# Performance work log

Measured on AMD Instinct MI355X. Metric: run time of the kernel, lower is better.

## Reference

```python
import jax, jax.numpy as jnp
import numpy as np

N = 100000
E = 3200000
IN_DIM = 128
OUT_DIM = 64


def setup_inputs() -> dict:
    key = jax.random.key(0)
    k1, k2, k3, k4, k5, k6 = jax.random.split(key, 6)
    x = jax.random.normal(k1, (N, IN_DIM), dtype=jnp.float32)
    edge_index = jax.random.randint(k2, (2, E), 0, N, dtype=jnp.int64)
    edge_weight = jax.random.uniform(k3, (E,), dtype=jnp.float32)
    # Learned params: Linear weight (in->out, no bias), attention vectors a_src/a_tgt
    limit_w = float(np.sqrt(1.0 / IN_DIM))
    W = jax.random.uniform(k4, (IN_DIM, OUT_DIM), minval=-limit_w, maxval=limit_w, dtype=jnp.float32)
    # xavier_uniform for (out_dim, 1) parameters
    limit_a = float(np.sqrt(6.0 / (OUT_DIM + 1)))
    a_src = jax.random.uniform(k5, (OUT_DIM,), minval=-limit_a, maxval=limit_a, dtype=jnp.float32)
    a_tgt = jax.random.uniform(k6, (OUT_DIM,), minval=-limit_a, maxval=limit_a, dtype=jnp.float32)
    return {"x": x, "edge_index": edge_index, "edge_weight": edge_weight,
            "W": W, "a_src": a_src, "a_tgt": a_tgt}


def reference(x, edge_index, edge_weight, W, a_src, a_tgt):
    n = x.shape[0]
    h = x @ W  # (N, out_dim)
    src, tgt = edge_index[0], edge_index[1]
    # per-node attention logits, gathered per edge
    hs = h @ a_src  # (N,)
    ht = h @ a_tgt  # (N,)
    e = jax.nn.leaky_relu(hs[src] + ht[tgt], negative_slope=0.2)  # (E,)
    e = e * edge_weight
    # segment softmax over incoming edges of each target node
    e_max = jax.ops.segment_max(e, tgt, num_segments=n)  # (N,), -inf for isolated nodes
    e_exp = jnp.exp(e - e_max[tgt])  # (E,)
    e_sum = jax.ops.segment_sum(e_exp, tgt, num_segments=n)  # (N,)
    alpha = e_exp / (e_sum[tgt] + 1e-10)  # (E,)
    # weighted scatter-add aggregation
    out = jax.ops.segment_sum(alpha[:, None] * h[src], tgt, num_segments=n)  # (N, out_dim)
    return out
```

## Files before the change

### kernel.cpp

```cpp
#include <hip/hip_runtime.h>


#define IN_DIM 128
#define OUT_DIM 64
#define MAXBKT 512
#define BKN 256
#define SEPT 8
#define SCHUNK (1024 * SEPT)
#define CAP 9216

typedef __attribute__((ext_vector_type(8))) short bf16x8;
typedef __attribute__((ext_vector_type(4))) float f32x4;

__device__ __forceinline__ unsigned short f2bf(float f) {
    unsigned u = __float_as_uint(f);
    return (unsigned short)((u + 0x7FFFu + ((u >> 16) & 1u)) >> 16);
}
__device__ __forceinline__ float bf2f(unsigned short u) {
    return __uint_as_float((unsigned)u << 16);
}

__device__ __forceinline__ float expg(float d) {
    return __expf(fmaxf(d, -80.f));
}

__global__ __launch_bounds__(256) void k_linear(
    const float* __restrict__ x, const float* __restrict__ W,
    const float* __restrict__ a_src, const float* __restrict__ a_tgt,
    unsigned short* __restrict__ hh, float* __restrict__ hs,
    float* __restrict__ ht, int n)
{
    __shared__ unsigned short xhi[64][136];
    __shared__ unsigned short xlo[64][136];
    __shared__ unsigned short whi[64][136];
    __shared__ unsigned short wlo[64][136];
    const int tid   = threadIdx.x;
    const int node0 = blockIdx.x * 64;

    {
        const float4* W4 = (const float4*)W;
        #pragma unroll
        for (int j = 0; j < 8; ++j) {
            int i4 = tid + 256 * j;
            int k = i4 >> 4, d4 = i4 & 15;
            float4 v = W4[i4];
            float vv[4] = {v.x, v.y, v.z, v.w};
            #pragma unroll
            for (int m = 0; m < 4; ++m) {
                unsigned short hi = f2bf(vv[m]);
                float lo = vv[m] - bf2f(hi);
                whi[d4 * 4 + m][k] = hi;
                wlo[d4 * 4 + m][k] = f2bf(lo);
            }
        }
    }
    {
        #pragma unroll
        for (int j = 0; j < 8; ++j) {
            int i4 = tid + 256 * j;
            int r = i4 >> 5, c4 = i4 & 31;
            int node = node0 + r;
            float4 v = make_float4(0.f, 0.f, 0.f, 0.f);
            if (node < n) v = ((const float4*)(x + (size_t)node * IN_DIM))[c4];
            float vv[4] = {v.x, v.y, v.z, v.w};
            ushort4 ph, pl;
            unsigned short* php = (unsigned short*)&ph;
            unsigned short* plp = (unsigned short*)&pl;
            #pragma unroll
            for (int m = 0; m < 4; ++m) {
                unsigned short hi = f2bf(vv[m]);
                php[m] = hi;
                plp[m] = f2bf(vv[m] - bf2f(hi));
            }
            *(ushort4*)&xhi[r][c4 * 4] = ph;
            *(ushort4*)&xlo[r][c4 * 4] = pl;
        }
    }
    __syncthreads();

    const int l15  = tid & 15;
    const int lhi  = (tid & 63) >> 4;
    const int wv   = tid >> 6;
    const int arow = wv * 16 + l15;
    const int kb   = lhi * 8;

    bf16x8 ahi[4], alo[4];
    #pragma unroll
    for (int k0 = 0; k0 < 4; ++k0) {
        ahi[k0] = *(const bf16x8*)&xhi[arow][k0 * 32 + kb];
        alo[k0] = *(const bf16x8*)&xlo[arow][k0 * 32 + kb];
    }

    f32x4 acc[4];
    #pragma unroll
    for (int ntt = 0; ntt < 4; ++ntt) acc[ntt] = (f32x4){0.f, 0.f, 0.f, 0.f};

    #pragma unroll
    for (int ntt = 0; ntt < 4; ++ntt) {
        #pragma unroll
        for (int k0 = 0; k0 < 4; ++k0) {
            bf16x8 bhi = *(const bf16x8*)&whi[ntt * 16 + l15][k0 * 32 + kb];
            bf16x8 blo = *(const bf16x8*)&wlo[ntt * 16 + l15][k0 * 32 + kb];
            acc[ntt] = __builtin_amdgcn_mfma_f32_16x16x32_bf16(ahi[k0], bhi, acc[ntt], 0, 0, 0);
            acc[ntt] = __builtin_amdgcn_mfma_f32_16x16x32_bf16(ahi[k0], blo, acc[ntt], 0, 0, 0);
            acc[ntt] = __builtin_amdgcn_mfma_f32_16x16x32_bf16(alo[k0], bhi, acc[ntt], 0, 0, 0);
        }
    }

    float asv[4], atv[4];
    #pragma unroll
    for (int ntt = 0; ntt < 4; ++ntt) {
        asv[ntt] = a_src[ntt * 16 + l15];
        atv[ntt] = a_tgt[ntt * 16 + l15];
    }
    #pragma unroll
    for (int q = 0; q < 4; ++q) {
        float ps = 0.f, pt = 0.f;
        #pragma unroll
        for (int ntt = 0; ntt < 4; ++ntt) {
            ps += acc[ntt][q] * asv[ntt];
            pt += acc[ntt][q] * atv[ntt];
        }
        #pragma unroll
        for (int off = 8; off; off >>= 1) {
            ps += __shfl_xor(ps, off);
            pt += __shfl_xor(pt, off);
        }
        int node = node0 + wv * 16 + lhi * 4 + q;
        if (l15 == 0 && node < n) { hs[node] = ps; ht[node] = pt; }
    }

    __syncthreads();
    #pragma unroll
    for (int ntt = 0; ntt < 4; ++ntt) {
        #pragma unroll
        for (int q = 0; q < 4; ++q) {
            xhi[wv * 16 + lhi * 4 + q][ntt * 16 + l15] = f2bf(acc[ntt][q]);
        }
    }
    __syncthreads();
    #pragma unroll
    for (int j = 0; j < 4; ++j) {
        int i = tid + 256 * j;
        int r = i >> 4, c4 = i & 15;
        int node = node0 + r;
        if (node < n) {
            ushort4 v = *(const ushort4*)&xhi[r][c4 * 4];
            ((ushort4*)(hh + (size_t)node * OUT_DIM))[c4] = v;
        }
    }
}

__global__ __launch_bounds__(1024) void k_count(
    const int* __restrict__ tgt, int* __restrict__ histT,
    int ecount, int nbkt, int nsb)
{
    __shared__ int h[MAXBKT];
    const int tid = threadIdx.x;
    const int e0  = blockIdx.x * SCHUNK;
    for (int i = tid; i < nbkt; i += 1024) h[i] = 0;
    __syncthreads();
    #pragma unroll
    for (int k = 0; k < SEPT; ++k) {
        int j = e0 + k * 1024 + tid;
        if (j < ecount) atomicAdd(&h[tgt[j] >> 8], 1);
    }
    __syncthreads();
    for (int i = tid; i < nbkt; i += 1024) histT[i * nsb + blockIdx.x] = h[i];
}

__global__ __launch_bounds__(512) void k_colscan(
    int* __restrict__ histT, int* __restrict__ bfill, int nsb)
{
    __shared__ int lds[512];
    const int bkt = blockIdx.x;
    const int tid = threadIdx.x;
    int v = (tid < nsb) ? histT[bkt * nsb + tid] : 0;
    lds[tid] = v;
    __syncthreads();
    for (int off = 1; off < 512; off <<= 1) {
        int u = (tid >= off) ? lds[tid - off] : 0;
        __syncthreads();
        lds[tid] += u;
        __syncthreads();
    }
    int excl = lds[tid] - v;
    if (tid < nsb) histT[bkt * nsb + tid] = bkt * CAP + excl;
    if (tid == 511) bfill[bkt] = bkt * CAP + lds[511];
}

__global__ __launch_bounds__(1024) void k_scat(
    const int* __restrict__ src, const int* __restrict__ tgt,
    const float* __restrict__ ew, const float* __restrict__ hs,
    const float* __restrict__ ht, const int* __restrict__ histT,
    float2* __restrict__ ecoarse, int ecount, int nbkt, int nsb)
{
    __shared__ int h[MAXBKT];
    __shared__ int base[MAXBKT];
    const int tid = threadIdx.x;
    const int e0  = blockIdx.x * SCHUNK;

    for (int i = tid; i < nbkt; i += 1024) {
        h[i] = 0;
        base[i] = histT[i * nsb + blockIdx.x];
    }

    unsigned kreg[SEPT]; int breg[SEPT]; float wreg[SEPT];
    #pragma unroll
    for (int k = 0; k < SEPT; ++k) {
        int j = e0 + k * 1024 + tid;
        bool valid = j < ecount;
        int s = valid ? src[j] : 0;
        int t = valid ? tgt[j] : 0;
        wreg[k] = valid ? ew[j] : 0.f;
        kreg[k] = ((unsigned)s << 8) | ((unsigned)t & 255u);
        breg[k] = t >> 8;
    }
    float hsr[SEPT], htr[SEPT];
    #pragma unroll
    for (int k = 0; k < SEPT; ++k) hsr[k] = hs[kreg[k] >> 8];
    #pragma unroll
    for (int k = 0; k < SEPT; ++k) htr[k] = ht[(breg[k] << 8) | (int)(kreg[k] & 255u)];

    __syncthreads();

    int rank[SEPT];
    #pragma unroll
    for (int k = 0; k < SEPT; ++k) {
        int j = e0 + k * 1024 + tid;
        if (j < ecount) rank[k] = atomicAdd(&h[breg[k]], 1);
    }

    #pragma unroll
    for (int k = 0; k < SEPT; ++k) {
        int j = e0 + k * 1024 + tid;
        if (j < ecount) {
            float v = hsr[k] + htr[k];
            v = (v > 0.f) ? v : 0.2f * v;
            v *= wreg[k];
            ecoarse[base[breg[k]] + rank[k]] = make_float2(__uint_as_float(kreg[k]), v);
        }
    }
}

__global__ __launch_bounds__(1024, 8) void k_bucket(
    const int* __restrict__ bfill, const float2* __restrict__ ecoarse,
    const unsigned short* __restrict__ hh, float* __restrict__ out, int n)
{
    __shared__ float2 recs[CAP];
    __shared__ int   cnt[BKN];
    __shared__ int   pos0[BKN];
    __shared__ int   fill[BKN];
    __shared__ float mf[BKN];
    __shared__ float rden[BKN];

    const int tid   = threadIdx.x;
    const int bkt   = blockIdx.x;
    const int base  = bkt * CAP;
    const int node0 = bkt << 8;
    const int mcnt  = bfill[bkt] - base;

    for (int i = tid; i < BKN; i += 1024) cnt[i] = 0;
    __syncthreads();

    for (int j = tid; j < mcnt; j += 1024) {
        unsigned k = __float_as_uint(ecoarse[base + j].x);
        atomicAdd(&cnt[k & 255u], 1);
    }
    __syncthreads();

    if (tid < BKN) pos0[tid] = cnt[tid];
    __syncthreads();
    for (int off = 1; off < BKN; off <<= 1) {
        int u = 0;
        if (tid < BKN && tid >= off) u = pos0[tid - off];
        __syncthreads();
        if (tid < BKN) pos0[tid] += u;
        __syncthreads();
    }
    if (tid < BKN) fill[tid] = pos0[tid] - cnt[tid];
    __syncthreads();
    if (tid < BKN) pos0[tid] = fill[tid];
    __syncthreads();

    for (int j = tid; j < mcnt; j += 1024) {
        float2 e = ecoarse[base + j];
        unsigned k = __float_as_uint(e.x);
        int p = atomicAdd(&fill[k & 255u], 1);
        recs[p] = e;
    }
    __syncthreads();

    {
        const int G   = tid >> 4;
        const int l16 = tid & 15;
        #pragma unroll
        for (int r = 0; r < 4; ++r) {
            int tl = G + 64 * r;
            int s0 = pos0[tl], c = cnt[tl];
            float m = -INFINITY, s = 0.f;
            for (int j = l16; j < c; j += 16) {
                float v = recs[s0 + j].y;
                float nm = fmaxf(m, v);
                s = s * expg(m - nm) + expg(v - nm);
                m = nm;
            }
            #pragma unroll
            for (int off = 8; off; off >>= 1) {
                float mo = __shfl_xor(m, off);
                float so = __shfl_xor(s, off);
                float nm = fmaxf(m, mo);
                s = s * expg(m - nm) + so * expg(mo - nm);
                m = nm;
            }
            if (l16 == 0) { mf[tl] = m; rden[tl] = 1.f / (s + 1e-10f); }
        }
    }
    __syncthreads();

    const int lane = tid & 63;
    const int wv   = tid >> 6;
    const int g    = lane >> 4;
    const int l4   = lane & 15;
    #pragma unroll 1
    for (int r = 0; r < 16; ++r) {
        int tl = wv + 16 * r;
        int node = node0 + tl;
        if (node >= n) continue;
        int s0 = pos0[tl], e_ = s0 + cnt[tl];
        float m = mf[tl], rd = rden[tl];
        float4 a0 = make_float4(0.f, 0.f, 0.f, 0.f);
        float4 a1 = make_float4(0.f, 0.f, 0.f, 0.f);
        int j = s0;
        for (; j + 8 <= e_; j += 8) {
            float2 e0 = recs[j + g];
            float2 e1 = recs[j + 4 + g];
            int sA = (int)(__float_as_uint(e0.x) >> 8);
            int sB = (int)(__float_as_uint(e1.x) >> 8);
            ushort4 u0 = ((const ushort4*)(hh + (size_t)sA * OUT_DIM))[l4];
            ushort4 u1 = ((const ushort4*)(hh + (size_t)sB * OUT_DIM))[l4];
            float c0 = __expf(e0.y - m) * rd;
            float c1 = __expf(e1.y - m) * rd;
            a0.x += c0 * bf2f(u0.x); a0.y += c0 * bf2f(u0.y);
            a0.z += c0 * bf2f(u0.z); a0.w += c0 * bf2f(u0.w);
            a1.x += c1 * bf2f(u1.x); a1.y += c1 * bf2f(u1.y);
            a1.z += c1 * bf2f(u1.z); a1.w += c1 * bf2f(u1.w);
        }
        for (; j < e_; j += 4) {
            int jj = j + g;
            bool valid = jj < e_;
            float2 ed = recs[valid ? jj : (e_ - 1)];
            int sidx = (int)(__float_as_uint(ed.x) >> 8);
            ushort4 uv = ((const ushort4*)(hh + (size_t)sidx * OUT_DIM))[l4];
            float c = valid ? __expf(ed.y - m) * rd : 0.f;
            a0.x += c * bf2f(uv.x); a0.y += c * bf2f(uv.y);
            a0.z += c * bf2f(uv.z); a0.w += c * bf2f(uv.w);
        }
        a0.x += a1.x; a0.y += a1.y; a0.z += a1.z; a0.w += a1.w;

        #pragma unroll
        for (int off = 32; off >= 16; off >>= 1) {
            a0.x += __shfl_xor(a0.x, off);
            a0.y += __shfl_xor(a0.y, off);
            a0.z += __shfl_xor(a0.z, off);
            a0.w += __shfl_xor(a0.w, off);
        }
        if (g == 0)
            ((float4*)(out + (size_t)node * OUT_DIM))[l4] = a0;
    }
}

extern "C" void kernel_launch(void* const* d_in, const int* in_sizes, int n_in,
                              void* d_out, int out_size, void* d_ws, size_t ws_size,
                              hipStream_t stream) {
    const float* x     = (const float*)d_in[0];
    const int*   eidx  = (const int*)d_in[1];
    const float* ew    = (const float*)d_in[2];
    const float* W     = (const float*)d_in[3];
    const float* a_src = (const float*)d_in[4];
    const float* a_tgt = (const float*)d_in[5];
    float* out = (float*)d_out;

    const int n = in_sizes[0] / IN_DIM;
    const int E = in_sizes[2];
    const int* src = eidx;
    const int* tgt = eidx + E;
    const int nbkt = (n + BKN - 1) / BKN;
    const int nsb  = (E + SCHUNK - 1) / SCHUNK;

    unsigned* ws = (unsigned*)d_ws;
    unsigned short* hh = (unsigned short*)ws;  ws += (size_t)n * OUT_DIM / 2;
    float* hs     = (float*)ws;          ws += n;
    float* ht     = (float*)ws;          ws += n;
    int*   bfill  = (int*)ws;            ws += MAXBKT;
    int*   histT  = (int*)ws;            ws += (size_t)nbkt * nsb;
    ws = (unsigned*)(((uintptr_t)ws + 7) & ~(uintptr_t)7);
    float2* ecoarse = (float2*)ws;

    k_linear<<<(n + 63) / 64, 256, 0, stream>>>(x, W, a_src, a_tgt, hh, hs, ht, n);
    k_count<<<nsb, 1024, 0, stream>>>(tgt, histT, E, nbkt, nsb);
    k_colscan<<<nbkt, 512, 0, stream>>>(histT, bfill, nsb);
    k_scat<<<nsb, 1024, 0, stream>>>(src, tgt, ew, hs, ht, histT, ecoarse, E, nbkt, nsb);
    k_bucket<<<nbkt, 1024, 0, stream>>>(bfill, ecoarse, hh, out, n);
}
```

Measured before the change: 271.3 us.

## Split each bucket across two half-blocks and precompute normalized softmax coefficients

```diff
diff --git a/kernel.cpp b/kernel.cpp
--- a/kernel.cpp
+++ b/kernel.cpp
@@ -5,9 +5,11 @@
 #define OUT_DIM 64
 #define MAXBKT 512
 #define BKN 256
+#define HBKN 128
 #define SEPT 8
 #define SCHUNK (1024 * SEPT)
 #define CAP 9216
+#define CAPL 4736
 
 typedef __attribute__((ext_vector_type(8))) short bf16x8;
 typedef __attribute__((ext_vector_type(4))) float f32x4;
@@ -243,51 +245,55 @@
     }
 }
 
-__global__ __launch_bounds__(1024, 8) void k_bucket(
+__global__ __launch_bounds__(512, 8) void k_half(
     const int* __restrict__ bfill, const float2* __restrict__ ecoarse,
     const unsigned short* __restrict__ hh, float* __restrict__ out, int n)
 {
-    __shared__ float2 recs[CAP];
-    __shared__ int   cnt[BKN];
-    __shared__ int   pos0[BKN];
-    __shared__ int   fill[BKN];
-    __shared__ float mf[BKN];
-    __shared__ float rden[BKN];
+    __shared__ float2 recs[CAPL];
+    __shared__ int   cnt[HBKN];
+    __shared__ int   pos0[HBKN];
+    __shared__ int   fill[HBKN];
+    __shared__ float mf[HBKN];
+    __shared__ float rden[HBKN];
 
     const int tid   = threadIdx.x;
-    const int bkt   = blockIdx.x;
+    const int B     = blockIdx.x;
+    const int bkt   = B >> 1;
+    const int hf    = B & 1;
     const int base  = bkt * CAP;
-    const int node0 = bkt << 8;
+    const int node0 = (bkt << 8) + (hf << 7);
     const int mcnt  = bfill[bkt] - base;
 
-    for (int i = tid; i < BKN; i += 1024) cnt[i] = 0;
-    __syncthreads();
-
-    for (int j = tid; j < mcnt; j += 1024) {
-        unsigned k = __float_as_uint(ecoarse[base + j].x);
-        atomicAdd(&cnt[k & 255u], 1);
-    }
-    __syncthreads();
-
-    if (tid < BKN) pos0[tid] = cnt[tid];
-    __syncthreads();
-    for (int off = 1; off < BKN; off <<= 1) {
+    for (int i = tid; i < HBKN; i += 512) cnt[i] = 0;
+    __syncthreads();
+
+    for (int j = tid; j < mcnt; j += 512) {
+        int tl = (int)(__float_as_uint(ecoarse[base + j].x) & 255u);
+        if ((tl >> 7) == hf) atomicAdd(&cnt[tl & 127], 1);
+    }
+    __syncthreads();
+
+    if (tid < HBKN) pos0[tid] = cnt[tid];
+    __syncthreads();
+    for (int off = 1; off < HBKN; off <<= 1) {
         int u = 0;
-        if (tid < BKN && tid >= off) u = pos0[tid - off];
+        if (tid < HBKN && tid >= off) u = pos0[tid - off];
         __syncthreads();
-        if (tid < BKN) pos0[tid] += u;
+        if (tid < HBKN) pos0[tid] += u;
         __syncthreads();
     }
-    if (tid < BKN) fill[tid] = pos0[tid] - cnt[tid];
-    __syncthreads();
-    if (tid < BKN) pos0[tid] = fill[tid];
-    __syncthreads();
-
-    for (int j = tid; j < mcnt; j += 1024) {
+    if (tid < HBKN) fill[tid] = pos0[tid] - cnt[tid];
+    __syncthreads();
+    if (tid < HBKN) pos0[tid] = fill[tid];
+    __syncthreads();
+
+    for (int j = tid; j < mcnt; j += 512) {
         float2 e = ecoarse[base + j];
-        unsigned k = __float_as_uint(e.x);
-        int p = atomicAdd(&fill[k & 255u], 1);
-        recs[p] = e;
+        int tl = (int)(__float_as_uint(e.x) & 255u);
+        if ((tl >> 7) == hf) {
+            int p = atomicAdd(&fill[tl & 127], 1);
+            if (p < CAPL) recs[p] = e;
+        }
     }
     __syncthreads();
 
@@ -296,7 +302,7 @@
         const int l16 = tid & 15;
         #pragma unroll
         for (int r = 0; r < 4; ++r) {
-            int tl = G + 64 * r;
+            int tl = G + 32 * r;
             int s0 = pos0[tl], c = cnt[tl];
             float m = -INFINITY, s = 0.f;
             for (int j = l16; j < c; j += 16) {
@@ -318,17 +324,25 @@
     }
     __syncthreads();
 
+    int ntot = fill[HBKN - 1];
+    if (ntot > CAPL) ntot = CAPL;
+    for (int j = tid; j < ntot; j += 512) {
+        float2 e = recs[j];
+        int tl = (int)(__float_as_uint(e.x) & 127u);
+        recs[j].y = __expf(e.y - mf[tl]) * rden[tl];
+    }
+    __syncthreads();
+
     const int lane = tid & 63;
     const int wv   = tid >> 6;
     const int g    = lane >> 4;
     const int l4   = lane & 15;
     #pragma unroll 1
     for (int r = 0; r < 16; ++r) {
-        int tl = wv + 16 * r;
+        int tl = wv + 8 * r;
         int node = node0 + tl;
         if (node >= n) continue;
         int s0 = pos0[tl], e_ = s0 + cnt[tl];
-        float m = mf[tl], rd = rden[tl];
         float4 a0 = make_float4(0.f, 0.f, 0.f, 0.f);
         float4 a1 = make_float4(0.f, 0.f, 0.f, 0.f);
         int j = s0;
@@ -339,8 +353,8 @@
             int sB = (int)(__float_as_uint(e1.x) >> 8);
             ushort4 u0 = ((const ushort4*)(hh + (size_t)sA * OUT_DIM))[l4];
             ushort4 u1 = ((const ushort4*)(hh + (size_t)sB * OUT_DIM))[l4];
-            float c0 = __expf(e0.y - m) * rd;
-            float c1 = __expf(e1.y - m) * rd;
+            float c0 = e0.y;
+            float c1 = e1.y;
             a0.x += c0 * bf2f(u0.x); a0.y += c0 * bf2f(u0.y);
             a0.z += c0 * bf2f(u0.z); a0.w += c0 * bf2f(u0.w);
             a1.x += c1 * bf2f(u1.x); a1.y += c1 * bf2f(u1.y);
@@ -352,7 +366,7 @@
             float2 ed = recs[valid ? jj : (e_ - 1)];
             int sidx = (int)(__float_as_uint(ed.x) >> 8);
             ushort4 uv = ((const ushort4*)(hh + (size_t)sidx * OUT_DIM))[l4];
-            float c = valid ? __expf(ed.y - m) * rd : 0.f;
+            float c = valid ? ed.y : 0.f;
             a0.x += c * bf2f(uv.x); a0.y += c * bf2f(uv.y);
             a0.z += c * bf2f(uv.z); a0.w += c * bf2f(uv.w);
         }
@@ -401,5 +415,5 @@
     k_count<<<nsb, 1024, 0, stream>>>(tgt, histT, E, nbkt, nsb);
     k_colscan<<<nbkt, 512, 0, stream>>>(histT, bfill, nsb);
     k_scat<<<nsb, 1024, 0, stream>>>(src, tgt, ew, hs, ht, histT, ecoarse, E, nbkt, nsb);
-    k_bucket<<<nbkt, 1024, 0, stream>>>(bfill, ecoarse, hh, out, n);
-}
+    k_half<<<2 * nbkt, 512, 0, stream>>>(bfill, ecoarse, hh, out, n);
+}
```

Result: slower. 278.5 us (+2.6%).

## Fuse all graph-attention stages into one cooperative persistent kernel with grid syncs

Applied to the files above, without the earlier changes.

```diff
diff --git a/kernel.cpp b/kernel.cpp
--- a/kernel.cpp
+++ b/kernel.cpp
@@ -1,4 +1,7 @@
 #include <hip/hip_runtime.h>
+#include <hip/hip_cooperative_groups.h>
+
+namespace cg = cooperative_groups;
 
 
 #define IN_DIM 128
@@ -19,275 +22,244 @@
 __device__ __forceinline__ float bf2f(unsigned short u) {
     return __uint_as_float((unsigned)u << 16);
 }
-
 __device__ __forceinline__ float expg(float d) {
     return __expf(fmaxf(d, -80.f));
 }
 
-__global__ __launch_bounds__(256) void k_linear(
-    const float* __restrict__ x, const float* __restrict__ W,
-    const float* __restrict__ a_src, const float* __restrict__ a_tgt,
-    unsigned short* __restrict__ hh, float* __restrict__ hs,
-    float* __restrict__ ht, int n)
-{
-    __shared__ unsigned short xhi[64][136];
-    __shared__ unsigned short xlo[64][136];
-    __shared__ unsigned short whi[64][136];
-    __shared__ unsigned short wlo[64][136];
-    const int tid   = threadIdx.x;
-    const int node0 = blockIdx.x * 64;
-
-    {
-        const float4* W4 = (const float4*)W;
-        #pragma unroll
-        for (int j = 0; j < 8; ++j) {
-            int i4 = tid + 256 * j;
+struct KParams {
+    const float* x; const float* W; const float* a_src; const float* a_tgt;
+    const int* src; const int* tgt; const float* ew;
+    unsigned short* hh; float* hs; float* ht;
+    int* bfill; int* histT; float2* ecoarse; float* out;
+    int n, ecount, nbkt, nsb, nlb;
+};
+
+union SharedU {
+    struct {
+        unsigned short whi[64][136], wlo[64][136];
+        unsigned short xhi[64][136], xlo[64][136];
+        float hsp[4][64], htp[4][64];
+    } lin;
+    struct { int h[MAXBKT]; int base[MAXBKT]; } cs;
+    struct { int lds[512]; } scan;
+    struct {
+        float2 recs[CAP];
+        int cnt[BKN], pos0[BKN], fill[BKN];
+        float mf[BKN], rden[BKN];
+    } bkt;
+};
+
+__device__ void phase_lin(const KParams& P, SharedU& su, int blk, int tid)
+{
+    auto& L = su.lin;
+    if (blk < P.nlb) {
+        const float4* W4 = (const float4*)P.W;
+        #pragma unroll
+        for (int j = 0; j < 2; ++j) {
+            int i4 = tid + 1024 * j;
             int k = i4 >> 4, d4 = i4 & 15;
             float4 v = W4[i4];
             float vv[4] = {v.x, v.y, v.z, v.w};
             #pragma unroll
             for (int m = 0; m < 4; ++m) {
                 unsigned short hi = f2bf(vv[m]);
-                float lo = vv[m] - bf2f(hi);
-                whi[d4 * 4 + m][k] = hi;
-                wlo[d4 * 4 + m][k] = f2bf(lo);
-            }
-        }
-    }
-    {
-        #pragma unroll
-        for (int j = 0; j < 8; ++j) {
-            int i4 = tid + 256 * j;
-            int r = i4 >> 5, c4 = i4 & 31;
-            int node = node0 + r;
-            float4 v = make_float4(0.f, 0.f, 0.f, 0.f);
-            if (node < n) v = ((const float4*)(x + (size_t)node * IN_DIM))[c4];
-            float vv[4] = {v.x, v.y, v.z, v.w};
-            ushort4 ph, pl;
-            unsigned short* php = (unsigned short*)&ph;
-            unsigned short* plp = (unsigned short*)&pl;
+                L.whi[d4 * 4 + m][k] = hi;
+                L.wlo[d4 * 4 + m][k] = f2bf(vv[m] - bf2f(hi));
+            }
+        }
+    }
+    const int lane = tid & 63, l15 = lane & 15, lhi = lane >> 4;
+    const int w = tid >> 6, rowgrp = w & 3, nt = w >> 2;
+    const int arow = rowgrp * 16 + l15, kb = lhi * 8;
+
+    for (int tt = 0; tt < 4; ++tt) {
+        const int node0 = blk * 256 + tt * 64;
+        const bool act = (blk < P.nlb) && (node0 < P.n);
+        __syncthreads();
+        if (act) {
             #pragma unroll
-            for (int m = 0; m < 4; ++m) {
-                unsigned short hi = f2bf(vv[m]);
-                php[m] = hi;
-                plp[m] = f2bf(vv[m] - bf2f(hi));
-            }
-            *(ushort4*)&xhi[r][c4 * 4] = ph;
-            *(ushort4*)&xlo[r][c4 * 4] = pl;
-        }
-    }
-    __syncthreads();
-
-    const int l15  = tid & 15;
-    const int lhi  = (tid & 63) >> 4;
-    const int wv   = tid >> 6;
-    const int arow = wv * 16 + l15;
-    const int kb   = lhi * 8;
-
-    bf16x8 ahi[4], alo[4];
-    #pragma unroll
-    for (int k0 = 0; k0 < 4; ++k0) {
-        ahi[k0] = *(const bf16x8*)&xhi[arow][k0 * 32 + kb];
-        alo[k0] = *(const bf16x8*)&xlo[arow][k0 * 32 + kb];
-    }
-
-    f32x4 acc[4];
-    #pragma unroll
-    for (int ntt = 0; ntt < 4; ++ntt) acc[ntt] = (f32x4){0.f, 0.f, 0.f, 0.f};
-
-    #pragma unroll
-    for (int ntt = 0; ntt < 4; ++ntt) {
-        #pragma unroll
-        for (int k0 = 0; k0 < 4; ++k0) {
-            bf16x8 bhi = *(const bf16x8*)&whi[ntt * 16 + l15][k0 * 32 + kb];
-            bf16x8 blo = *(const bf16x8*)&wlo[ntt * 16 + l15][k0 * 32 + kb];
-            acc[ntt] = __builtin_amdgcn_mfma_f32_16x16x32_bf16(ahi[k0], bhi, acc[ntt], 0, 0, 0);
-            acc[ntt] = __builtin_amdgcn_mfma_f32_16x16x32_bf16(ahi[k0], blo, acc[ntt], 0, 0, 0);
-            acc[ntt] = __builtin_amdgcn_mfma_f32_16x16x32_bf16(alo[k0], bhi, acc[ntt], 0, 0, 0);
-        }
-    }
-
-    float asv[4], atv[4];
-    #pragma unroll
-    for (int ntt = 0; ntt < 4; ++ntt) {
-        asv[ntt] = a_src[ntt * 16 + l15];
-        atv[ntt] = a_tgt[ntt * 16 + l15];
-    }
-    #pragma unroll
-    for (int q = 0; q < 4; ++q) {
-        float ps = 0.f, pt = 0.f;
-        #pragma unroll
-        for (int ntt = 0; ntt < 4; ++ntt) {
-            ps += acc[ntt][q] * asv[ntt];
-            pt += acc[ntt][q] * atv[ntt];
-        }
-        #pragma unroll
-        for (int off = 8; off; off >>= 1) {
-            ps += __shfl_xor(ps, off);
-            pt += __shfl_xor(pt, off);
-        }
-        int node = node0 + wv * 16 + lhi * 4 + q;
-        if (l15 == 0 && node < n) { hs[node] = ps; ht[node] = pt; }
-    }
-
-    __syncthreads();
-    #pragma unroll
-    for (int ntt = 0; ntt < 4; ++ntt) {
-        #pragma unroll
-        for (int q = 0; q < 4; ++q) {
-            xhi[wv * 16 + lhi * 4 + q][ntt * 16 + l15] = f2bf(acc[ntt][q]);
-        }
-    }
-    __syncthreads();
-    #pragma unroll
-    for (int j = 0; j < 4; ++j) {
-        int i = tid + 256 * j;
-        int r = i >> 4, c4 = i & 15;
-        int node = node0 + r;
-        if (node < n) {
-            ushort4 v = *(const ushort4*)&xhi[r][c4 * 4];
-            ((ushort4*)(hh + (size_t)node * OUT_DIM))[c4] = v;
-        }
-    }
-}
-
-__global__ __launch_bounds__(1024) void k_count(
-    const int* __restrict__ tgt, int* __restrict__ histT,
-    int ecount, int nbkt, int nsb)
-{
-    __shared__ int h[MAXBKT];
-    const int tid = threadIdx.x;
-    const int e0  = blockIdx.x * SCHUNK;
-    for (int i = tid; i < nbkt; i += 1024) h[i] = 0;
-    __syncthreads();
+            for (int j = 0; j < 2; ++j) {
+                int i4 = tid + 1024 * j;
+                int r = i4 >> 5, c4 = i4 & 31;
+                int node = node0 + r;
+                float4 v = make_float4(0.f, 0.f, 0.f, 0.f);
+                if (node < P.n) v = ((const float4*)(P.x + (size_t)node * IN_DIM))[c4];
+                float vv[4] = {v.x, v.y, v.z, v.w};
+                ushort4 ph, pl;
+                unsigned short* php = (unsigned short*)&ph;
+                unsigned short* plp = (unsigned short*)&pl;
+                #pragma unroll
+                for (int m = 0; m < 4; ++m) {
+                    unsigned short hi = f2bf(vv[m]);
+                    php[m] = hi;
+                    plp[m] = f2bf(vv[m] - bf2f(hi));
+                }
+                *(ushort4*)&L.xhi[r][c4 * 4] = ph;
+                *(ushort4*)&L.xlo[r][c4 * 4] = pl;
+            }
+        }
+        __syncthreads();
+        if (act) {
+            f32x4 acc = (f32x4){0.f, 0.f, 0.f, 0.f};
+            #pragma unroll
+            for (int k0 = 0; k0 < 4; ++k0) {
+                bf16x8 ahi = *(const bf16x8*)&L.xhi[arow][k0 * 32 + kb];
+                bf16x8 alo = *(const bf16x8*)&L.xlo[arow][k0 * 32 + kb];
+                bf16x8 bhi = *(const bf16x8*)&L.whi[nt * 16 + l15][k0 * 32 + kb];
+                bf16x8 blo = *(const bf16x8*)&L.wlo[nt * 16 + l15][k0 * 32 + kb];
+                acc = __builtin_amdgcn_mfma_f32_16x16x32_bf16(ahi, bhi, acc, 0, 0, 0);
+                acc = __builtin_amdgcn_mfma_f32_16x16x32_bf16(ahi, blo, acc, 0, 0, 0);
+                acc = __builtin_amdgcn_mfma_f32_16x16x32_bf16(alo, bhi, acc, 0, 0, 0);
+            }
+            float asv = P.a_src[nt * 16 + l15];
+            float atv = P.a_tgt[nt * 16 + l15];
+            #pragma unroll
+            for (int q = 0; q < 4; ++q) {
+                float ps = acc[q] * asv, pt = acc[q] * atv;
+                #pragma unroll
+                for (int off = 8; off; off >>= 1) {
+                    ps += __shfl_xor(ps, off);
+                    pt += __shfl_xor(pt, off);
+                }
+                int rit = rowgrp * 16 + lhi * 4 + q;
+                if (l15 == 0) { L.hsp[nt][rit] = ps; L.htp[nt][rit] = pt; }
+                int node = node0 + rit;
+                if (node < P.n)
+                    P.hh[(size_t)node * OUT_DIM + nt * 16 + l15] = f2bf(acc[q]);
+            }
+        }
+        __syncthreads();
+        if (act && tid < 64) {
+            int node = node0 + tid;
+            if (node < P.n) {
+                P.hs[node] = L.hsp[0][tid] + L.hsp[1][tid] + L.hsp[2][tid] + L.hsp[3][tid];
+                P.ht[node] = L.htp[0][tid] + L.htp[1][tid] + L.htp[2][tid] + L.htp[3][tid];
+            }
+        }
+    }
+}
+
+__device__ void phase_count(const KParams& P, SharedU& su, int blk, int tid)
+{
+    if (blk >= P.nsb) return;
+    auto& C = su.cs;
+    for (int i = tid; i < P.nbkt; i += 1024) C.h[i] = 0;
+    __syncthreads();
+    const int e0 = blk * SCHUNK;
     #pragma unroll
     for (int k = 0; k < SEPT; ++k) {
         int j = e0 + k * 1024 + tid;
-        if (j < ecount) atomicAdd(&h[tgt[j] >> 8], 1);
-    }
-    __syncthreads();
-    for (int i = tid; i < nbkt; i += 1024) histT[i * nsb + blockIdx.x] = h[i];
-}
-
-__global__ __launch_bounds__(512) void k_colscan(
-    int* __restrict__ histT, int* __restrict__ bfill, int nsb)
-{
-    __shared__ int lds[512];
-    const int bkt = blockIdx.x;
-    const int tid = threadIdx.x;
-    int v = (tid < nsb) ? histT[bkt * nsb + tid] : 0;
-    lds[tid] = v;
+        if (j < P.ecount) atomicAdd(&C.h[P.tgt[j] >> 8], 1);
+    }
+    __syncthreads();
+    for (int i = tid; i < P.nbkt; i += 1024) P.histT[i * P.nsb + blk] = C.h[i];
+}
+
+__device__ void phase_scan(const KParams& P, SharedU& su, int blk, int tid)
+{
+    if (blk >= P.nbkt) return;
+    int v = 0;
+    if (tid < 512) {
+        v = (tid < P.nsb) ? P.histT[blk * P.nsb + tid] : 0;
+        su.scan.lds[tid] = v;
+    }
     __syncthreads();
     for (int off = 1; off < 512; off <<= 1) {
-        int u = (tid >= off) ? lds[tid - off] : 0;
-        __syncthreads();
-        lds[tid] += u;
-        __syncthreads();
-    }
-    int excl = lds[tid] - v;
-    if (tid < nsb) histT[bkt * nsb + tid] = bkt * CAP + excl;
-    if (tid == 511) bfill[bkt] = bkt * CAP + lds[511];
-}
-
-__global__ __launch_bounds__(1024) void k_scat(
-    const int* __restrict__ src, const int* __restrict__ tgt,
-    const float* __restrict__ ew, const float* __restrict__ hs,
-    const float* __restrict__ ht, const int* __restrict__ histT,
-    float2* __restrict__ ecoarse, int ecount, int nbkt, int nsb)
-{
-    __shared__ int h[MAXBKT];
-    __shared__ int base[MAXBKT];
-    const int tid = threadIdx.x;
-    const int e0  = blockIdx.x * SCHUNK;
-
-    for (int i = tid; i < nbkt; i += 1024) {
-        h[i] = 0;
-        base[i] = histT[i * nsb + blockIdx.x];
-    }
-
-    unsigned kreg[SEPT]; int breg[SEPT]; float wreg[SEPT];
-    #pragma unroll
-    for (int k = 0; k < SEPT; ++k) {
-        int j = e0 + k * 1024 + tid;
-        bool valid = j < ecount;
-        int s = valid ? src[j] : 0;
-        int t = valid ? tgt[j] : 0;
-        wreg[k] = valid ? ew[j] : 0.f;
-        kreg[k] = ((unsigned)s << 8) | ((unsigned)t & 255u);
-        breg[k] = t >> 8;
-    }
-    float hsr[SEPT], htr[SEPT];
-    #pragma unroll
-    for (int k = 0; k < SEPT; ++k) hsr[k] = hs[kreg[k] >> 8];
-    #pragma unroll
-    for (int k = 0; k < SEPT; ++k) htr[k] = ht[(breg[k] << 8) | (int)(kreg[k] & 255u)];
-
-    __syncthreads();
-
-    int rank[SEPT];
-    #pragma unroll
-    for (int k = 0; k < SEPT; ++k) {
-        int j = e0 + k * 1024 + tid;
-        if (j < ecount) rank[k] = atomicAdd(&h[breg[k]], 1);
-    }
-
-    #pragma unroll
-    for (int k = 0; k < SEPT; ++k) {
-        int j = e0 + k * 1024 + tid;
-        if (j < ecount) {
-            float v = hsr[k] + htr[k];
-            v = (v > 0.f) ? v : 0.2f * v;
-            v *= wreg[k];
-            ecoarse[base[breg[k]] + rank[k]] = make_float2(__uint_as_float(kreg[k]), v);
-        }
-    }
-}
-
-__global__ __launch_bounds__(1024, 8) void k_bucket(
-    const int* __restrict__ bfill, const float2* __restrict__ ecoarse,
-    const unsigned short* __restrict__ hh, float* __restrict__ out, int n)
-{
-    __shared__ float2 recs[CAP];
-    __shared__ int   cnt[BKN];
-    __shared__ int   pos0[BKN];
-    __shared__ int   fill[BKN];
-    __shared__ float mf[BKN];
-    __shared__ float rden[BKN];
-
-    const int tid   = threadIdx.x;
-    const int bkt   = blockIdx.x;
-    const int base  = bkt * CAP;
-    const int node0 = bkt << 8;
-    const int mcnt  = bfill[bkt] - base;
-
-    for (int i = tid; i < BKN; i += 1024) cnt[i] = 0;
+        int u = (tid < 512 && tid >= off) ? su.scan.lds[tid - off] : 0;
+        __syncthreads();
+        if (tid < 512) su.scan.lds[tid] += u;
+        __syncthreads();
+    }
+    if (tid < P.nsb) P.histT[blk * P.nsb + tid] = blk * CAP + (su.scan.lds[tid] - v);
+    if (tid == 511) P.bfill[blk] = blk * CAP + su.scan.lds[511];
+}
+
+__device__ void phase_scat(const KParams& P, SharedU& su, int blk, int tid)
+{
+    if (blk >= P.nsb) return;
+    auto& C = su.cs;
+    for (int i = tid; i < P.nbkt; i += 1024) {
+        C.h[i] = 0;
+        C.base[i] = P.histT[i * P.nsb + blk];
+    }
+    __syncthreads();
+    const int e0 = blk * SCHUNK;
+    #pragma unroll 1
+    for (int half = 0; half < 2; ++half) {
+        const int eh = e0 + half * 4096;
+        unsigned kreg[4]; int breg[4]; float wreg[4];
+        #pragma unroll
+        for (int k = 0; k < 4; ++k) {
+            int j = eh + k * 1024 + tid;
+            bool valid = j < P.ecount;
+            int s = valid ? P.src[j] : 0;
+            int t = valid ? P.tgt[j] : 0;
+            wreg[k] = valid ? P.ew[j] : 0.f;
+            kreg[k] = ((unsigned)s << 8) | ((unsigned)t & 255u);
+            breg[k] = t >> 8;
+        }
+        float hsr[4], htr[4];
+        #pragma unroll
+        for (int k = 0; k < 4; ++k) hsr[k] = P.hs[kreg[k] >> 8];
+        #pragma unroll
+        for (int k = 0; k < 4; ++k) htr[k] = P.ht[(breg[k] << 8) | (int)(kreg[k] & 255u)];
+        int rank[4];
+        #pragma unroll
+        for (int k = 0; k < 4; ++k) {
+            int j = eh + k * 1024 + tid;
+            if (j < P.ecount) rank[k] = atomicAdd(&C.h[breg[k]], 1);
+        }
+        #pragma unroll
+        for (int k = 0; k < 4; ++k) {
+            int j = eh + k * 1024 + tid;
+            if (j < P.ecount) {
+                float v = hsr[k] + htr[k];
+                v = (v > 0.f) ? v : 0.2f * v;
+                v *= wreg[k];
+                P.ecoarse[C.base[breg[k]] + rank[k]] =
+                    make_float2(__uint_as_float(kreg[k]), v);
+            }
+        }
+    }
+}
+
+__device__ void phase_bkt(const KParams& P, SharedU& su, int blk, int tid)
+{
+    if (blk >= P.nbkt) return;
+    auto& B = su.bkt;
+    const int base  = blk * CAP;
+    const int node0 = blk << 8;
+    int mcnt = P.bfill[blk] - base;
+    if (mcnt > CAP) mcnt = CAP;
+
+    for (int i = tid; i < BKN; i += 1024) B.cnt[i] = 0;
     __syncthreads();
 
     for (int j = tid; j < mcnt; j += 1024) {
-        unsigned k = __float_as_uint(ecoarse[base + j].x);
-        atomicAdd(&cnt[k & 255u], 1);
-    }
-    __syncthreads();
-
-    if (tid < BKN) pos0[tid] = cnt[tid];
+        unsigned k = __float_as_uint(P.ecoarse[base + j].x);
+        atomicAdd(&B.cnt[k & 255u], 1);
+    }
+    __syncthreads();
+
+    if (tid < BKN) B.pos0[tid] = B.cnt[tid];
     __syncthreads();
     for (int off = 1; off < BKN; off <<= 1) {
         int u = 0;
-        if (tid < BKN && tid >= off) u = pos0[tid - off];
-        __syncthreads();
-        if (tid < BKN) pos0[tid] += u;
-        __syncthreads();
-    }
-    if (tid < BKN) fill[tid] = pos0[tid] - cnt[tid];
-    __syncthreads();
-    if (tid < BKN) pos0[tid] = fill[tid];
+        if (tid < BKN && tid >= off) u = B.pos0[tid - off];
+        __syncthreads();
+        if (tid < BKN) B.pos0[tid] += u;
+        __syncthreads();
+    }
+    if (tid < BKN) B.fill[tid] = B.pos0[tid] - B.cnt[tid];
+    __syncthreads();
+    if (tid < BKN) B.pos0[tid] = B.fill[tid];
     __syncthreads();
 
     for (int j = tid; j < mcnt; j += 1024) {
-        float2 e = ecoarse[base + j];
+        float2 e = P.ecoarse[base + j];
         unsigned k = __float_as_uint(e.x);
-        int p = atomicAdd(&fill[k & 255u], 1);
-        recs[p] = e;
+        int p = atomicAdd(&B.fill[k & 255u], 1);
+        if (p < CAP) B.recs[p] = e;
     }
     __syncthreads();
 
@@ -297,10 +269,10 @@
         #pragma unroll
         for (int r = 0; r < 4; ++r) {
             int tl = G + 64 * r;
-            int s0 = pos0[tl], c = cnt[tl];
+            int s0 = B.pos0[tl], c = B.cnt[tl];
             float m = -INFINITY, s = 0.f;
             for (int j = l16; j < c; j += 16) {
-                float v = recs[s0 + j].y;
+                float v = B.recs[s0 + j].y;
                 float nm = fmaxf(m, v);
                 s = s * expg(m - nm) + expg(v - nm);
                 m = nm;
@@ -313,8 +285,17 @@
                 s = s * expg(m - nm) + so * expg(mo - nm);
                 m = nm;
             }
-            if (l16 == 0) { mf[tl] = m; rden[tl] = 1.f / (s + 1e-10f); }
-        }
+            if (l16 == 0) { B.mf[tl] = m; B.rden[tl] = 1.f / (s + 1e-10f); }
+        }
+    }
+    __syncthreads();
+
+    int ntot = B.fill[BKN - 1];
+    if (ntot > CAP) ntot = CAP;
+    for (int j = tid; j < ntot; j += 1024) {
+        float2 e = B.recs[j];
+        int tl = (int)(__float_as_uint(e.x) & 255u);
+        B.recs[j].y = __expf(e.y - B.mf[tl]) * B.rden[tl];
     }
     __syncthreads();
 
@@ -326,21 +307,19 @@
     for (int r = 0; r < 16; ++r) {
         int tl = wv + 16 * r;
         int node = node0 + tl;
-        if (node >= n) continue;
-        int s0 = pos0[tl], e_ = s0 + cnt[tl];
-        float m = mf[tl], rd = rden[tl];
+        if (node >= P.n) continue;
+        int s0 = B.pos0[tl], e_ = s0 + B.cnt[tl];
         float4 a0 = make_float4(0.f, 0.f, 0.f, 0.f);
         float4 a1 = make_float4(0.f, 0.f, 0.f, 0.f);
         int j = s0;
         for (; j + 8 <= e_; j += 8) {
-            float2 e0 = recs[j + g];
-            float2 e1 = recs[j + 4 + g];
+            float2 e0 = B.recs[j + g];
+            float2 e1 = B.recs[j + 4 + g];
             int sA = (int)(__float_as_uint(e0.x) >> 8);
             int sB = (int)(__float_as_uint(e1.x) >> 8);
-            ushort4 u0 = ((const ushort4*)(hh + (size_t)sA * OUT_DIM))[l4];
-            ushort4 u1 = ((const ushort4*)(hh + (size_t)sB * OUT_DIM))[l4];
-            float c0 = __expf(e0.y - m) * rd;
-            float c1 = __expf(e1.y - m) * rd;
+            ushort4 u0 = ((const ushort4*)(P.hh + (size_t)sA * OUT_DIM))[l4];
+            ushort4 u1 = ((const ushort4*)(P.hh + (size_t)sB * OUT_DIM))[l4];
+            float c0 = e0.y, c1 = e1.y;
             a0.x += c0 * bf2f(u0.x); a0.y += c0 * bf2f(u0.y);
             a0.z += c0 * bf2f(u0.z); a0.w += c0 * bf2f(u0.w);
             a1.x += c1 * bf2f(u1.x); a1.y += c1 * bf2f(u1.y);
@@ -349,15 +328,14 @@
         for (; j < e_; j += 4) {
             int jj = j + g;
             bool valid = jj < e_;
-            float2 ed = recs[valid ? jj : (e_ - 1)];
+            float2 ed = B.recs[valid ? jj : (e_ - 1)];
             int sidx = (int)(__float_as_uint(ed.x) >> 8);
-            ushort4 uv = ((const ushort4*)(hh + (size_t)sidx * OUT_DIM))[l4];
-            float c = valid ? __expf(ed.y - m) * rd : 0.f;
+            ushort4 uv = ((const ushort4*)(P.hh + (size_t)sidx * OUT_DIM))[l4];
+            float c = valid ? ed.y : 0.f;
             a0.x += c * bf2f(uv.x); a0.y += c * bf2f(uv.y);
             a0.z += c * bf2f(uv.z); a0.w += c * bf2f(uv.w);
         }
         a0.x += a1.x; a0.y += a1.y; a0.z += a1.z; a0.w += a1.w;
-
         #pragma unroll
         for (int off = 32; off >= 16; off >>= 1) {
             a0.x += __shfl_xor(a0.x, off);
@@ -366,9 +344,34 @@
             a0.w += __shfl_xor(a0.w, off);
         }
         if (g == 0)
-            ((float4*)(out + (size_t)node * OUT_DIM))[l4] = a0;
-    }
-}
+            ((float4*)(P.out + (size_t)node * OUT_DIM))[l4] = a0;
+    }
+}
+
+__global__ __launch_bounds__(1024, 8) void k_fused(KParams P)
+{
+    __shared__ SharedU su;
+    cg::grid_group grid = cg::this_grid();
+    const int tid = threadIdx.x;
+    const int blk = blockIdx.x;
+
+    phase_lin(P, su, blk, tid);
+    __syncthreads();
+    phase_count(P, su, blk, tid);
+    grid.sync();
+    phase_scan(P, su, blk, tid);
+    grid.sync();
+    phase_scat(P, su, blk, tid);
+    grid.sync();
+    __syncthreads();
+    phase_bkt(P, su, blk, tid);
+}
+
+__global__ __launch_bounds__(1024, 8) void k_p0(KParams P) { __shared__ SharedU su; phase_lin(P, su, blockIdx.x, threadIdx.x); }
+__global__ __launch_bounds__(1024, 8) void k_p1(KParams P) { __shared__ SharedU su; phase_count(P, su, blockIdx.x, threadIdx.x); }
+__global__ __launch_bounds__(1024, 8) void k_p2(KParams P) { __shared__ SharedU su; phase_scan(P, su, blockIdx.x, threadIdx.x); }
+__global__ __launch_bounds__(1024, 8) void k_p3(KParams P) { __shared__ SharedU su; phase_scat(P, su, blockIdx.x, threadIdx.x); }
+__global__ __launch_bounds__(1024, 8) void k_p4(KParams P) { __shared__ SharedU su; phase_bkt(P, su, blockIdx.x, threadIdx.x); }
 
 extern "C" void kernel_launch(void* const* d_in, const int* in_sizes, int n_in,
                               void* d_out, int out_size, void* d_ws, size_t ws_size,
@@ -383,10 +386,12 @@
 
     const int n = in_sizes[0] / IN_DIM;
     const int E = in_sizes[2];
-    const int* src = eidx;
-    const int* tgt = eidx + E;
     const int nbkt = (n + BKN - 1) / BKN;
     const int nsb  = (E + SCHUNK - 1) / SCHUNK;
+    const int nlb  = (n + 255) / 256;
+    int nblk = nbkt;
+    if (nsb > nblk) nblk = nsb;
+    if (nlb > nblk) nblk = nlb;
 
     unsigned* ws = (unsigned*)d_ws;
     unsigned short* hh = (unsigned short*)ws;  ws += (size_t)n * OUT_DIM / 2;
@@ -397,9 +402,21 @@
     ws = (unsigned*)(((uintptr_t)ws + 7) & ~(uintptr_t)7);
     float2* ecoarse = (float2*)ws;
 
-    k_linear<<<(n + 63) / 64, 256, 0, stream>>>(x, W, a_src, a_tgt, hh, hs, ht, n);
-    k_count<<<nsb, 1024, 0, stream>>>(tgt, histT, E, nbkt, nsb);
-    k_colscan<<<nbkt, 512, 0, stream>>>(histT, bfill, nsb);
-    k_scat<<<nsb, 1024, 0, stream>>>(src, tgt, ew, hs, ht, histT, ecoarse, E, nbkt, nsb);
-    k_bucket<<<nbkt, 1024, 0, stream>>>(bfill, ecoarse, hh, out, n);
-}
+    KParams P;
+    P.x = x; P.W = W; P.a_src = a_src; P.a_tgt = a_tgt;
+    P.src = eidx; P.tgt = eidx + E; P.ew = ew;
+    P.hh = hh; P.hs = hs; P.ht = ht;
+    P.bfill = bfill; P.histT = histT; P.ecoarse = ecoarse; P.out = out;
+    P.n = n; P.ecount = E; P.nbkt = nbkt; P.nsb = nsb; P.nlb = nlb;
+
+    void* kargs[] = { (void*)&P };
+    hipError_t err = hipLaunchCooperativeKernel(
+        (const void*)k_fused, dim3(nblk), dim3(1024), kargs, 0, stream);
+    if (err != hipSuccess) {
+        k_p0<<<nlb,  1024, 0, stream>>>(P);
+        k_p1<<<nsb,  1024, 0, stream>>>(P);
+        k_p2<<<nbkt, 1024, 0, stream>>>(P);
+        k_p3<<<nsb,  1024, 0, stream>>>(P);
+        k_p4<<<nbkt, 1024, 0, stream>>>(P);
+    }
+}
```

Measured after the change: 461.4 us. +70.1%, slower.

## Stage bucket scatter in LDS, precompute alpha, unroll gather deeper

Applied to the files above, without the earlier changes.

```diff
diff --git a/kernel.cpp b/kernel.cpp
--- a/kernel.cpp
+++ b/kernel.cpp
@@ -19,7 +19,6 @@
 __device__ __forceinline__ float bf2f(unsigned short u) {
     return __uint_as_float((unsigned)u << 16);
 }
-
 __device__ __forceinline__ float expg(float d) {
     return __expf(fmaxf(d, -80.f));
 }
@@ -48,9 +47,8 @@
             #pragma unroll
             for (int m = 0; m < 4; ++m) {
                 unsigned short hi = f2bf(vv[m]);
-                float lo = vv[m] - bf2f(hi);
                 whi[d4 * 4 + m][k] = hi;
-                wlo[d4 * 4 + m][k] = f2bf(lo);
+                wlo[d4 * 4 + m][k] = f2bf(vv[m] - bf2f(hi));
             }
         }
     }
@@ -195,14 +193,16 @@
     const float* __restrict__ ht, const int* __restrict__ histT,
     float2* __restrict__ ecoarse, int ecount, int nbkt, int nsb)
 {
-    __shared__ int h[MAXBKT];
-    __shared__ int base[MAXBKT];
+    __shared__ float2 recs[SCHUNK];
+    __shared__ int hcnt[MAXBKT];
+    __shared__ int lstart[MAXBKT];
+    __shared__ int gbase[MAXBKT];
     const int tid = threadIdx.x;
     const int e0  = blockIdx.x * SCHUNK;
 
     for (int i = tid; i < nbkt; i += 1024) {
-        h[i] = 0;
-        base[i] = histT[i * nsb + blockIdx.x];
+        hcnt[i]  = 0;
+        gbase[i] = histT[i * nsb + blockIdx.x];
     }
 
     unsigned kreg[SEPT]; int breg[SEPT]; float wreg[SEPT];
@@ -221,6 +221,13 @@
     for (int k = 0; k < SEPT; ++k) hsr[k] = hs[kreg[k] >> 8];
     #pragma unroll
     for (int k = 0; k < SEPT; ++k) htr[k] = ht[(breg[k] << 8) | (int)(kreg[k] & 255u)];
+    float ereg[SEPT];
+    #pragma unroll
+    for (int k = 0; k < SEPT; ++k) {
+        float v = hsr[k] + htr[k];
+        v = (v > 0.f) ? v : 0.2f * v;
+        ereg[k] = v * wreg[k];
+    }
 
     __syncthreads();
 
@@ -228,18 +235,41 @@
     #pragma unroll
     for (int k = 0; k < SEPT; ++k) {
         int j = e0 + k * 1024 + tid;
-        if (j < ecount) rank[k] = atomicAdd(&h[breg[k]], 1);
-    }
+        if (j < ecount) rank[k] = atomicAdd(&hcnt[breg[k]], 1);
+    }
+    __syncthreads();
+
+    int v = 0;
+    if (tid < 512) {
+        v = (tid < nbkt) ? hcnt[tid] : 0;
+        lstart[tid] = v;
+    }
+    __syncthreads();
+    for (int off = 1; off < 512; off <<= 1) {
+        int u = 0;
+        if (tid < 512 && tid >= off) u = lstart[tid - off];
+        __syncthreads();
+        if (tid < 512) lstart[tid] += u;
+        __syncthreads();
+    }
+    if (tid < 512) lstart[tid] -= v;
+    __syncthreads();
 
     #pragma unroll
     for (int k = 0; k < SEPT; ++k) {
         int j = e0 + k * 1024 + tid;
-        if (j < ecount) {
-            float v = hsr[k] + htr[k];
-            v = (v > 0.f) ? v : 0.2f * v;
-            v *= wreg[k];
-            ecoarse[base[breg[k]] + rank[k]] = make_float2(__uint_as_float(kreg[k]), v);
-        }
+        if (j < ecount)
+            recs[lstart[breg[k]] + rank[k]] =
+                make_float2(__uint_as_float(kreg[k]), ereg[k]);
+    }
+    __syncthreads();
+
+    const int wv   = tid >> 6;
+    const int lane = tid & 63;
+    for (int b = wv; b < nbkt; b += 16) {
+        int st = lstart[b], c = hcnt[b], gb = gbase[b];
+        for (int i = lane; i < c; i += 64)
+            ecoarse[gb + i] = recs[st + i];
     }
 }
 
@@ -258,7 +288,8 @@
     const int bkt   = blockIdx.x;
     const int base  = bkt * CAP;
     const int node0 = bkt << 8;
-    const int mcnt  = bfill[bkt] - base;
+    int mcnt = bfill[bkt] - base;
+    if (mcnt > CAP) mcnt = CAP;
 
     for (int i = tid; i < BKN; i += 1024) cnt[i] = 0;
     __syncthreads();
@@ -287,7 +318,7 @@
         float2 e = ecoarse[base + j];
         unsigned k = __float_as_uint(e.x);
         int p = atomicAdd(&fill[k & 255u], 1);
-        recs[p] = e;
+        if (p < CAP) recs[p] = e;
     }
     __syncthreads();
 
@@ -318,6 +349,13 @@
     }
     __syncthreads();
 
+    for (int j = tid; j < mcnt; j += 1024) {
+        float2 e = recs[j];
+        int tl = (int)(__float_as_uint(e.x) & 255u);
+        recs[j].y = __expf(e.y - mf[tl]) * rden[tl];
+    }
+    __syncthreads();
+
     const int lane = tid & 63;
     const int wv   = tid >> 6;
     const int g    = lane >> 4;
@@ -328,10 +366,32 @@
         int node = node0 + tl;
         if (node >= n) continue;
         int s0 = pos0[tl], e_ = s0 + cnt[tl];
-        float m = mf[tl], rd = rden[tl];
         float4 a0 = make_float4(0.f, 0.f, 0.f, 0.f);
         float4 a1 = make_float4(0.f, 0.f, 0.f, 0.f);
         int j = s0;
+        for (; j + 16 <= e_; j += 16) {
+            float2 e0 = recs[j + g];
+            float2 e1 = recs[j + 4 + g];
+            float2 e2 = recs[j + 8 + g];
+            float2 e3 = recs[j + 12 + g];
+            int sA = (int)(__float_as_uint(e0.x) >> 8);
+            int sB = (int)(__float_as_uint(e1.x) >> 8);
+            int sC = (int)(__float_as_uint(e2.x) >> 8);
+            int sD = (int)(__float_as_uint(e3.x) >> 8);
+            ushort4 u0 = ((const ushort4*)(hh + (size_t)sA * OUT_DIM))[l4];
+            ushort4 u1 = ((const ushort4*)(hh + (size_t)sB * OUT_DIM))[l4];
+            ushort4 u2 = ((const ushort4*)(hh + (size_t)sC * OUT_DIM))[l4];
+            ushort4 u3 = ((const ushort4*)(hh + (size_t)sD * OUT_DIM))[l4];
+            float c0 = e0.y, c1 = e1.y, c2 = e2.y, c3 = e3.y;
+            a0.x += c0 * bf2f(u0.x); a0.y += c0 * bf2f(u0.y);
+            a0.z += c0 * bf2f(u0.z); a0.w += c0 * bf2f(u0.w);
+            a1.x += c1 * bf2f(u1.x); a1.y += c1 * bf2f(u1.y);
+            a1.z += c1 * bf2f(u1.z); a1.w += c1 * bf2f(u1.w);
+            a0.x += c2 * bf2f(u2.x); a0.y += c2 * bf2f(u2.y);
+            a0.z += c2 * bf2f(u2.z); a0.w += c2 * bf2f(u2.w);
+            a1.x += c3 * bf2f(u3.x); a1.y += c3 * bf2f(u3.y);
+            a1.z += c3 * bf2f(u3.z); a1.w += c3 * bf2f(u3.w);
+        }
         for (; j + 8 <= e_; j += 8) {
             float2 e0 = recs[j + g];
             float2 e1 = recs[j + 4 + g];
@@ -339,8 +399,7 @@
             int sB = (int)(__float_as_uint(e1.x) >> 8);
             ushort4 u0 = ((const ushort4*)(hh + (size_t)sA * OUT_DIM))[l4];
             ushort4 u1 = ((const ushort4*)(hh + (size_t)sB * OUT_DIM))[l4];
-            float c0 = __expf(e0.y - m) * rd;
-            float c1 = __expf(e1.y - m) * rd;
+            float c0 = e0.y, c1 = e1.y;
             a0.x += c0 * bf2f(u0.x); a0.y += c0 * bf2f(u0.y);
             a0.z += c0 * bf2f(u0.z); a0.w += c0 * bf2f(u0.w);
             a1.x += c1 * bf2f(u1.x); a1.y += c1 * bf2f(u1.y);
@@ -352,12 +411,11 @@
             float2 ed = recs[valid ? jj : (e_ - 1)];
             int sidx = (int)(__float_as_uint(ed.x) >> 8);
             ushort4 uv = ((const ushort4*)(hh + (size_t)sidx * OUT_DIM))[l4];
-            float c = valid ? __expf(ed.y - m) * rd : 0.f;
+            float c = valid ? ed.y : 0.f;
             a0.x += c * bf2f(uv.x); a0.y += c * bf2f(uv.y);
             a0.z += c * bf2f(uv.z); a0.w += c * bf2f(uv.w);
         }
         a0.x += a1.x; a0.y += a1.y; a0.z += a1.z; a0.w += a1.w;
-
         #pragma unroll
         for (int off = 32; off >= 16; off >>= 1) {
             a0.x += __shfl_xor(a0.x, off);
```

Result: no change. 267.2 us (median of 2 runs) (-1.5%).
